# Kernel optimization log

Measured on AMD Instinct MI355X. Metric: run time of the kernel, lower is better.

## Reference

```python
import jax, jax.numpy as jnp
import numpy as np

C = 256; HEADS = 8; LEVELS = 4; POINTS = 4; D = C // HEADS
SPATIAL = np.array([[96, 96], [48, 48], [24, 24], [12, 12]], dtype=np.int32)  # (H, W) per level
AREAS = SPATIAL[:, 0] * SPATIAL[:, 1]
HW = int(AREAS.sum())  # 12240
LSI = np.concatenate([[0], np.cumsum(AREAS)[:-1]]).astype(np.int32)
N = 1; Q = HW


def setup_inputs() -> dict:
    key = jax.random.key(0)
    ks = jax.random.split(key, 12)
    s = 0.02
    return {
        "query": jax.random.normal(ks[0], (N, Q, C), jnp.float32),
        "reference_points": jax.random.uniform(ks[1], (N, Q, LEVELS, 2), jnp.float32),
        "input_flatten": jax.random.normal(ks[2], (N, HW, C), jnp.float32),
        "input_spatial_shapes": jnp.asarray(SPATIAL),
        "input_level_start_index": jnp.asarray(LSI),
        "W_off": jax.random.normal(ks[3], (C, HEADS * LEVELS * POINTS * 2), jnp.float32) * s,
        "b_off": jax.random.normal(ks[4], (HEADS * LEVELS * POINTS * 2,), jnp.float32) * s,
        "W_attn": jax.random.normal(ks[5], (C, HEADS * LEVELS * POINTS), jnp.float32) * s,
        "b_attn": jax.random.normal(ks[6], (HEADS * LEVELS * POINTS,), jnp.float32) * s,
        "W_val": jax.random.normal(ks[7], (C, C), jnp.float32) * (1.0 / np.sqrt(C)),
        "b_val": jax.random.normal(ks[8], (C,), jnp.float32) * s,
        "W_out": jax.random.normal(ks[9], (C, C), jnp.float32) * (1.0 / np.sqrt(C)),
        "b_out": jax.random.normal(ks[10], (C,), jnp.float32) * s,
    }


def _ms_deform_attn(query, reference_points, input_flatten, sp, lsi,
                    W_off, b_off, W_attn, b_attn, W_val, b_val, W_out, b_out):
    n, q, c = query.shape
    hw = input_flatten.shape[1]
    # value projection -> [N, Hd, HW, D]
    value = (input_flatten @ W_val + b_val).reshape(n, hw, HEADS, D).transpose(0, 2, 1, 3)
    # sampling offsets [N,Q,Hd,L,P,2]
    off = (query @ W_off + b_off).reshape(n, q, HEADS, LEVELS, POINTS, 2)
    # attention weights softmaxed over L*P (done inside the fused CUDA kernel)
    attn = jax.nn.softmax((query @ W_attn + b_attn).reshape(n, q, HEADS, LEVELS * POINTS), axis=-1)
    attn = attn.reshape(n, q, HEADS, LEVELS, POINTS)
    # normalized sampling locations (reference_points last dim == 2 branch)
    norm = jnp.stack([sp[:, 1], sp[:, 0]], -1).astype(query.dtype)  # (W, H) per level
    loc = reference_points[:, :, None, :, None, :] + off / norm[None, None, None, :, None, :]
    Hl = sp[:, 0][None, None, None, :, None]
    Wl = sp[:, 1][None, None, None, :, None]
    start = lsi[None, None, None, :, None]
    # grid_sample-style (align_corners=False) pixel coordinates
    x = loc[..., 0] * Wl - 0.5
    y = loc[..., 1] * Hl - 0.5
    x0 = jnp.floor(x); y0 = jnp.floor(y)
    lx = x - x0; ly = y - y0
    x0i = x0.astype(jnp.int32); y0i = y0.astype(jnp.int32)

    def gather(yi, xi):
        valid = (xi >= 0) & (xi < Wl) & (yi >= 0) & (yi < Hl)
        idx = jnp.where(valid, start + yi * Wl + xi, 0)  # [N,Q,Hd,L,P]
        idx_t = idx.transpose(0, 2, 1, 3, 4).reshape(n, HEADS, q * LEVELS * POINTS, 1)
        g = jnp.take_along_axis(value, idx_t, axis=2)  # [N,Hd,Q*L*P,D]
        g = g.reshape(n, HEADS, q, LEVELS, POINTS, D)
        return g * valid.transpose(0, 2, 1, 3, 4)[..., None]

    def w(a):
        return a.transpose(0, 2, 1, 3, 4)[..., None]  # [N,Hd,Q,L,P,1]

    sampled = (gather(y0i, x0i) * w((1 - ly) * (1 - lx))
               + gather(y0i, x0i + 1) * w((1 - ly) * lx)
               + gather(y0i + 1, x0i) * w(ly * (1 - lx))
               + gather(y0i + 1, x0i + 1) * w(ly * lx))  # [N,Hd,Q,L,P,D]
    out = jnp.einsum('nhqlpd,nqhlp->nqhd', sampled, attn).reshape(n, q, c)
    return out @ W_out + b_out


def reference(query, reference_points, input_flatten, input_spatial_shapes, input_level_start_index,
              W_off, b_off, W_attn, b_attn, W_val, b_val, W_out, b_out):
    return _ms_deform_attn(query, reference_points, input_flatten,
                           input_spatial_shapes, input_level_start_index,
                           W_off, b_off, W_attn, b_attn, W_val, b_val, W_out, b_out)
```

## Files before the change

kernel.cpp:

```cpp
#include <hip/hip_runtime.h>

#define QTOT 12240
#define KD   256

typedef float f32x4 __attribute__((ext_vector_type(4)));
typedef short s16x8 __attribute__((ext_vector_type(8)));
typedef unsigned short ushort_t;

__device__ __forceinline__ unsigned short f2b(float x) {
    union { float f; unsigned u; } c; c.f = x;
    unsigned r = c.u + 0x7fffu + ((c.u >> 16) & 1u);
    return (unsigned short)(r >> 16);
}
__device__ __forceinline__ int swz(int row, int kb) { return row * 512 + (kb ^ ((row & 7) << 4)); }

__global__ __launch_bounds__(256) void prep(
    const float* __restrict__ W_val, const float* __restrict__ W_off,
    const float* __restrict__ W_attn, const float* __restrict__ W_out,
    const float* __restrict__ b_off, const float* __restrict__ b_attn,
    ushort_t* __restrict__ WvT, ushort_t* __restrict__ WcT,
    ushort_t* __restrict__ WoT, float* __restrict__ bcomb)
{
    int id = blockIdx.x * 256 + threadIdx.x;
    if (id < 65536) { int n = id >> 8, k = id & 255; WvT[id] = f2b(W_val[k * 256 + n]); }
    else if (id < 163840) {
        int t = id - 65536; int n = t >> 8, k = t & 255;
        float v = (n < 256) ? W_off[k * 256 + n] : W_attn[k * 128 + (n - 256)];
        WcT[t] = f2b(v);
    } else if (id < 229376) {
        int t = id - 163840; int n = t >> 8, k = t & 255;
        WoT[t] = f2b(W_out[k * 256 + n]);
    } else if (id < 229760) {
        int t = id - 229376; bcomb[t] = (t < 256) ? b_off[t] : b_attn[t - 256];
    }
}

__global__ __launch_bounds__(256) void gemm1(
    const float* __restrict__ inflat, const float* __restrict__ query,
    const ushort_t* __restrict__ WvT, const ushort_t* __restrict__ WcT,
    const float* __restrict__ b_val, const float* __restrict__ bcomb,
    ushort_t* __restrict__ projb, ushort_t* __restrict__ offb,
    float* __restrict__ logitf)
{
    __shared__ char As[16384];
    const int b = blockIdx.x;
    const bool isval = b < 383;
    const int bm = (isval ? b : b - 383) * 32;
    const float* A = isval ? inflat : query;
    const ushort_t* WT = isval ? WvT : WcT;
    const int nc = isval ? 4 : 6;

    const int tid = threadIdx.x, lane = tid & 63, wave = tid >> 6;
    const int lr = lane & 15, g8 = (lane >> 4) * 8;

    {
        const int row = tid >> 3, c0 = (tid & 7) * 32;
        const int grow = bm + row;
        if (grow < QTOT) {
            const float4* src = (const float4*)(A + (size_t)grow * KD + c0);
#pragma unroll
            for (int j = 0; j < 4; ++j) {
                float4 f0 = src[j * 2 + 0], f1 = src[j * 2 + 1];
                s16x8 v;
                v[0] = f2b(f0.x); v[1] = f2b(f0.y); v[2] = f2b(f0.z); v[3] = f2b(f0.w);
                v[4] = f2b(f1.x); v[5] = f2b(f1.y); v[6] = f2b(f1.z); v[7] = f2b(f1.w);
                *(s16x8*)(As + swz(row, (c0 + j * 8) * 2)) = v;
            }
        } else {
            s16x8 z = (s16x8)0;
#pragma unroll
            for (int j = 0; j < 4; ++j)
                *(s16x8*)(As + swz(row, (c0 + j * 8) * 2)) = z;
        }
    }
    __syncthreads();

    const int rg = (lane >> 4) * 4;

    for (int c = 0; c < nc; ++c) {
        const int col = c * 64 + wave * 16 + lr;
        s16x8 bfr[8];
        {
            const ushort_t* bp = WT + (size_t)col * KD + g8;
#pragma unroll
            for (int kc = 0; kc < 8; ++kc) bfr[kc] = *(const s16x8*)(bp + kc * 32);
        }
        f32x4 acc[2];
        acc[0] = (f32x4)0.f; acc[1] = (f32x4)0.f;
#pragma unroll
        for (int kc = 0; kc < 8; ++kc) {
            const int kb = (kc * 32 + g8) * 2;
            s16x8 a0 = *(const s16x8*)(As + swz(lr,      kb));
            s16x8 a1 = *(const s16x8*)(As + swz(16 + lr, kb));
            acc[0] = __builtin_amdgcn_mfma_f32_16x16x32_bf16(a0, bfr[kc], acc[0], 0, 0, 0);
            acc[1] = __builtin_amdgcn_mfma_f32_16x16x32_bf16(a1, bfr[kc], acc[1], 0, 0, 0);
        }
        const float bb = isval ? b_val[col] : bcomb[col];
#pragma unroll
        for (int mf = 0; mf < 2; ++mf)
#pragma unroll
            for (int rr = 0; rr < 4; ++rr) {
                const int row = bm + mf * 16 + rg + rr;
                if (row >= QTOT) continue;
                const float v = acc[mf][rr] + bb;
                if (isval)          projb[(size_t)row * 256 + col] = f2b(v);
                else if (col < 256) offb [(size_t)row * 256 + col] = f2b(v);
                else                logitf[(size_t)row * 128 + col - 256] = v;
            }
    }
}

__global__ __launch_bounds__(512) void sample_o(
    const float* __restrict__ rp, const ushort_t* __restrict__ offb,
    const float* __restrict__ logitf, const ushort_t* __restrict__ projb,
    const int* __restrict__ sp, const int* __restrict__ lsi,
    const ushort_t* __restrict__ WoT, const float* __restrict__ b_out,
    float* __restrict__ out)
{
    __shared__ int   s_idx[1024][4];
    __shared__ float s_w[1024][4];
    __shared__ char  outp[16384];

    const int bid = blockIdx.x;
    const int bm = bid * 32;
    const int tid = threadIdx.x;

    for (int sb = 0; sb < 4; ++sb) {
        const int qloc0 = sb * 8;
#pragma unroll
        for (int rep = 0; rep < 2; ++rep) {
            const int task = rep * 512 + tid;
            const int ql = task >> 7, t = task & 127;
            const int l = (t >> 2) & 3;
            int q = bm + qloc0 + ql;
            const int qc = (q < QTOT) ? q : (QTOT - 1);

            float logit = logitf[(size_t)qc * 128 + t];
            float mx = logit;
#pragma unroll
            for (int d = 1; d < 16; d <<= 1) mx = fmaxf(mx, __shfl_xor(mx, d));
            float e = __expf(logit - mx);
            float s = e;
#pragma unroll
            for (int d = 1; d < 16; d <<= 1) s += __shfl_xor(s, d);
            const float aw = e / s;

            const unsigned opk = *(const unsigned*)&offb[(size_t)qc * 256 + t * 2];
            const float ox = __uint_as_float(opk << 16);
            const float oy = __uint_as_float(opk & 0xffff0000u);

            const int Hl = sp[l * 2], Wl = sp[l * 2 + 1], st = lsi[l];
            const float rx = rp[((size_t)qc * 4 + l) * 2 + 0];
            const float ry = rp[((size_t)qc * 4 + l) * 2 + 1];

            const float x = rx * (float)Wl + ox - 0.5f;
            const float y = ry * (float)Hl + oy - 0.5f;
            const float xf = floorf(x), yf = floorf(y);
            const int x0 = (int)xf, y0 = (int)yf;
            const float lx = x - xf, ly = y - yf;

            const bool vx0 = (x0 >= 0) && (x0 < Wl);
            const bool vx1 = (x0 + 1 >= 0) && (x0 + 1 < Wl);
            const bool vy0 = (y0 >= 0) && (y0 < Hl);
            const bool vy1 = (y0 + 1 >= 0) && (y0 + 1 < Hl);

            s_w[task][0] = (vx0 && vy0) ? aw * (1.f - ly) * (1.f - lx) : 0.f;
            s_w[task][1] = (vx1 && vy0) ? aw * (1.f - ly) * lx         : 0.f;
            s_w[task][2] = (vx0 && vy1) ? aw * ly * (1.f - lx)         : 0.f;
            s_w[task][3] = (vx1 && vy1) ? aw * ly * lx                 : 0.f;
            s_idx[task][0] = (vx0 && vy0) ? (st + y0 * Wl + x0) * 512           : 0;
            s_idx[task][1] = (vx1 && vy0) ? (st + y0 * Wl + x0 + 1) * 512       : 0;
            s_idx[task][2] = (vx0 && vy1) ? (st + (y0 + 1) * Wl + x0) * 512     : 0;
            s_idx[task][3] = (vx1 && vy1) ? (st + (y0 + 1) * Wl + x0 + 1) * 512 : 0;
        }
        __syncthreads();

        {
            const int t = tid & 127, qlA = tid >> 7;
            const int h = t >> 4, pq = (t >> 2) & 3, c8 = t & 3;
            const char* basec = (const char*)projb + (h * 32 + c8 * 8) * 2;

            float aA[8] = {0,0,0,0,0,0,0,0};
            float aB[8] = {0,0,0,0,0,0,0,0};
#pragma unroll
            for (int l = 0; l < 4; ++l) {
                const int slotA = (qlA << 7)       + h * 16 + l * 4 + pq;
                const int slotB = ((qlA + 4) << 7) + h * 16 + l * 4 + pq;
                const int4   iA = *(const int4*)s_idx[slotA];
                const float4 wA = *(const float4*)s_w[slotA];
                const int4   iB = *(const int4*)s_idx[slotB];
                const float4 wB = *(const float4*)s_w[slotB];
#pragma unroll
                for (int c = 0; c < 4; ++c) {
                    const int   idA = (c == 0) ? iA.x : (c == 1) ? iA.y : (c == 2) ? iA.z : iA.w;
                    const float wwA = (c == 0) ? wA.x : (c == 1) ? wA.y : (c == 2) ? wA.z : wA.w;
                    const uint4 v = *(const uint4*)(basec + idA);
                    aA[0] += wwA * __uint_as_float(v.x << 16);
                    aA[1] += wwA * __uint_as_float(v.x & 0xffff0000u);
                    aA[2] += wwA * __uint_as_float(v.y << 16);
                    aA[3] += wwA * __uint_as_float(v.y & 0xffff0000u);
                    aA[4] += wwA * __uint_as_float(v.z << 16);
                    aA[5] += wwA * __uint_as_float(v.z & 0xffff0000u);
                    aA[6] += wwA * __uint_as_float(v.w << 16);
                    aA[7] += wwA * __uint_as_float(v.w & 0xffff0000u);
                }
#pragma unroll
                for (int c = 0; c < 4; ++c) {
                    const int   idB = (c == 0) ? iB.x : (c == 1) ? iB.y : (c == 2) ? iB.z : iB.w;
                    const float wwB = (c == 0) ? wB.x : (c == 1) ? wB.y : (c == 2) ? wB.z : wB.w;
                    const uint4 v = *(const uint4*)(basec + idB);
                    aB[0] += wwB * __uint_as_float(v.x << 16);
                    aB[1] += wwB * __uint_as_float(v.x & 0xffff0000u);
                    aB[2] += wwB * __uint_as_float(v.y << 16);
                    aB[3] += wwB * __uint_as_float(v.y & 0xffff0000u);
                    aB[4] += wwB * __uint_as_float(v.z << 16);
                    aB[5] += wwB * __uint_as_float(v.z & 0xffff0000u);
                    aB[6] += wwB * __uint_as_float(v.w << 16);
                    aB[7] += wwB * __uint_as_float(v.w & 0xffff0000u);
                }
            }
#pragma unroll
            for (int i = 0; i < 8; ++i) {
                aA[i] += __shfl_xor(aA[i], 4);  aA[i] += __shfl_xor(aA[i], 8);
                aB[i] += __shfl_xor(aB[i], 4);  aB[i] += __shfl_xor(aB[i], 8);
            }
            if (pq == 0) {
                const int colb = (h * 32 + c8 * 8) * 2;
                uint4 o;
                o.x = (unsigned)f2b(aA[0]) | ((unsigned)f2b(aA[1]) << 16);
                o.y = (unsigned)f2b(aA[2]) | ((unsigned)f2b(aA[3]) << 16);
                o.z = (unsigned)f2b(aA[4]) | ((unsigned)f2b(aA[5]) << 16);
                o.w = (unsigned)f2b(aA[6]) | ((unsigned)f2b(aA[7]) << 16);
                *(uint4*)(outp + swz(qloc0 + qlA, colb)) = o;
                o.x = (unsigned)f2b(aB[0]) | ((unsigned)f2b(aB[1]) << 16);
                o.y = (unsigned)f2b(aB[2]) | ((unsigned)f2b(aB[3]) << 16);
                o.z = (unsigned)f2b(aB[4]) | ((unsigned)f2b(aB[5]) << 16);
                o.w = (unsigned)f2b(aB[6]) | ((unsigned)f2b(aB[7]) << 16);
                *(uint4*)(outp + swz(qloc0 + qlA + 4, colb)) = o;
            }
        }
        __syncthreads();
    }

    const int lane = tid & 63, wave = tid >> 6;
    const int lr = lane & 15, g8 = (lane >> 4) * 8, rg = (lane >> 4) * 4;

    s16x8 bfr[2][8];
#pragma unroll
    for (int nf = 0; nf < 2; ++nf) {
        const ushort_t* bp = WoT + (size_t)(wave * 32 + nf * 16 + lr) * KD + g8;
#pragma unroll
        for (int kc = 0; kc < 8; ++kc) bfr[nf][kc] = *(const s16x8*)(bp + kc * 32);
    }

    f32x4 acc[2][2];
    acc[0][0] = (f32x4)0.f; acc[0][1] = (f32x4)0.f;
    acc[1][0] = (f32x4)0.f; acc[1][1] = (f32x4)0.f;
#pragma unroll
    for (int kc = 0; kc < 8; ++kc) {
        const int kb = (kc * 32 + g8) * 2;
        s16x8 a0 = *(const s16x8*)(outp + swz(lr,      kb));
        s16x8 a1 = *(const s16x8*)(outp + swz(16 + lr, kb));
        acc[0][0] = __builtin_amdgcn_mfma_f32_16x16x32_bf16(a0, bfr[0][kc], acc[0][0], 0, 0, 0);
        acc[1][0] = __builtin_amdgcn_mfma_f32_16x16x32_bf16(a1, bfr[0][kc], acc[1][0], 0, 0, 0);
        acc[0][1] = __builtin_amdgcn_mfma_f32_16x16x32_bf16(a0, bfr[1][kc], acc[0][1], 0, 0, 0);
        acc[1][1] = __builtin_amdgcn_mfma_f32_16x16x32_bf16(a1, bfr[1][kc], acc[1][1], 0, 0, 0);
    }

#pragma unroll
    for (int nf = 0; nf < 2; ++nf) {
        const int col = wave * 32 + nf * 16 + lr;
        const float bb = b_out[col];
#pragma unroll
        for (int mf = 0; mf < 2; ++mf)
#pragma unroll
            for (int rr = 0; rr < 4; ++rr) {
                const int row = bm + mf * 16 + rg + rr;
                if (row < QTOT) out[(size_t)row * 256 + col] = acc[mf][nf][rr] + bb;
            }
    }
}

extern "C" void kernel_launch(void* const* d_in, const int* in_sizes, int n_in,
                              void* d_out, int out_size, void* d_ws, size_t ws_size,
                              hipStream_t stream) {
    const float* query  = (const float*)d_in[0];
    const float* rp     = (const float*)d_in[1];
    const float* inflat = (const float*)d_in[2];
    const int*   sp     = (const int*)d_in[3];
    const int*   lsi    = (const int*)d_in[4];
    const float* W_off  = (const float*)d_in[5];
    const float* b_off  = (const float*)d_in[6];
    const float* W_attn = (const float*)d_in[7];
    const float* b_attn = (const float*)d_in[8];
    const float* W_val  = (const float*)d_in[9];
    const float* b_val  = (const float*)d_in[10];
    const float* W_out  = (const float*)d_in[11];
    const float* b_out  = (const float*)d_in[12];
    float* out = (float*)d_out;

    char* ws = (char*)d_ws;
    ushort_t* projb  = (ushort_t*)ws; ws += (size_t)QTOT * 256 * 2;
    ushort_t* offb   = (ushort_t*)ws; ws += (size_t)QTOT * 256 * 2;
    float*    logitf = (float*)ws;    ws += (size_t)QTOT * 128 * 4;
    ushort_t* WvT    = (ushort_t*)ws; ws += 65536 * 2;
    ushort_t* WcT    = (ushort_t*)ws; ws += 98304 * 2;
    ushort_t* WoT    = (ushort_t*)ws; ws += 65536 * 2;
    float*    bcomb  = (float*)ws;    ws += 384 * 4;

    prep<<<dim3(898), dim3(256), 0, stream>>>(W_val, W_off, W_attn, W_out, b_off, b_attn,
                                              WvT, WcT, WoT, bcomb);

    gemm1<<<dim3(766), dim3(256), 0, stream>>>(inflat, query, WvT, WcT, b_val, bcomb,
                                               projb, offb, logitf);

    sample_o<<<dim3(383), dim3(512), 0, stream>>>(rp, offb, logitf, projb, sp, lsi,
                                                  WoT, b_out, out);
}
```

Before: 82.24 us.

## Split sampling from output GEMM into separate kernels with finer-grained blocks

```diff
diff --git a/kernel.cpp b/kernel.cpp
--- a/kernel.cpp
+++ b/kernel.cpp
@@ -5,6 +5,7 @@
 
 typedef float f32x4 __attribute__((ext_vector_type(4)));
 typedef short s16x8 __attribute__((ext_vector_type(8)));
+typedef short s16x4 __attribute__((ext_vector_type(4)));
 typedef unsigned short ushort_t;
 
 __device__ __forceinline__ unsigned short f2b(float x) {
@@ -54,23 +55,18 @@
     const int lr = lane & 15, g8 = (lane >> 4) * 8;
 
     {
-        const int row = tid >> 3, c0 = (tid & 7) * 32;
-        const int grow = bm + row;
-        if (grow < QTOT) {
-            const float4* src = (const float4*)(A + (size_t)grow * KD + c0);
-#pragma unroll
-            for (int j = 0; j < 4; ++j) {
-                float4 f0 = src[j * 2 + 0], f1 = src[j * 2 + 1];
-                s16x8 v;
-                v[0] = f2b(f0.x); v[1] = f2b(f0.y); v[2] = f2b(f0.z); v[3] = f2b(f0.w);
-                v[4] = f2b(f1.x); v[5] = f2b(f1.y); v[6] = f2b(f1.z); v[7] = f2b(f1.w);
-                *(s16x8*)(As + swz(row, (c0 + j * 8) * 2)) = v;
-            }
-        } else {
-            s16x8 z = (s16x8)0;
-#pragma unroll
-            for (int j = 0; j < 4; ++j)
-                *(s16x8*)(As + swz(row, (c0 + j * 8) * 2)) = z;
+        const float4* srcb = (const float4*)(A + (size_t)bm * KD);
+        const int rem_rows = QTOT - bm;
+#pragma unroll
+        for (int j = 0; j < 8; ++j) {
+            const int f4i = j * 256 + tid;
+            const int row = f4i >> 6;
+            const int colb = (f4i & 63) * 8;
+            float4 f = make_float4(0.f, 0.f, 0.f, 0.f);
+            if (row < rem_rows) f = srcb[f4i];
+            s16x4 v;
+            v[0] = f2b(f.x); v[1] = f2b(f.y); v[2] = f2b(f.z); v[3] = f2b(f.w);
+            *(s16x4*)(As + swz(row, colb)) = v;
         }
     }
     __syncthreads();
@@ -110,173 +106,172 @@
     }
 }
 
-__global__ __launch_bounds__(512) void sample_o(
+__global__ __launch_bounds__(256) void sample5(
     const float* __restrict__ rp, const ushort_t* __restrict__ offb,
     const float* __restrict__ logitf, const ushort_t* __restrict__ projb,
     const int* __restrict__ sp, const int* __restrict__ lsi,
-    const ushort_t* __restrict__ WoT, const float* __restrict__ b_out,
-    float* __restrict__ out)
+    ushort_t* __restrict__ outpre)
 {
-    __shared__ int   s_idx[1024][4];
-    __shared__ float s_w[1024][4];
-    __shared__ char  outp[16384];
-
-    const int bid = blockIdx.x;
-    const int bm = bid * 32;
+    const int q0 = blockIdx.x * 4;
     const int tid = threadIdx.x;
 
-    for (int sb = 0; sb < 4; ++sb) {
-        const int qloc0 = sb * 8;
-#pragma unroll
-        for (int rep = 0; rep < 2; ++rep) {
-            const int task = rep * 512 + tid;
-            const int ql = task >> 7, t = task & 127;
-            const int l = (t >> 2) & 3;
-            int q = bm + qloc0 + ql;
-            const int qc = (q < QTOT) ? q : (QTOT - 1);
-
-            float logit = logitf[(size_t)qc * 128 + t];
-            float mx = logit;
-#pragma unroll
-            for (int d = 1; d < 16; d <<= 1) mx = fmaxf(mx, __shfl_xor(mx, d));
-            float e = __expf(logit - mx);
-            float s = e;
-#pragma unroll
-            for (int d = 1; d < 16; d <<= 1) s += __shfl_xor(s, d);
-            const float aw = e / s;
-
-            const unsigned opk = *(const unsigned*)&offb[(size_t)qc * 256 + t * 2];
-            const float ox = __uint_as_float(opk << 16);
-            const float oy = __uint_as_float(opk & 0xffff0000u);
-
-            const int Hl = sp[l * 2], Wl = sp[l * 2 + 1], st = lsi[l];
-            const float rx = rp[((size_t)qc * 4 + l) * 2 + 0];
-            const float ry = rp[((size_t)qc * 4 + l) * 2 + 1];
-
-            const float x = rx * (float)Wl + ox - 0.5f;
-            const float y = ry * (float)Hl + oy - 0.5f;
-            const float xf = floorf(x), yf = floorf(y);
-            const int x0 = (int)xf, y0 = (int)yf;
-            const float lx = x - xf, ly = y - yf;
-
-            const bool vx0 = (x0 >= 0) && (x0 < Wl);
-            const bool vx1 = (x0 + 1 >= 0) && (x0 + 1 < Wl);
-            const bool vy0 = (y0 >= 0) && (y0 < Hl);
-            const bool vy1 = (y0 + 1 >= 0) && (y0 + 1 < Hl);
-
-            s_w[task][0] = (vx0 && vy0) ? aw * (1.f - ly) * (1.f - lx) : 0.f;
-            s_w[task][1] = (vx1 && vy0) ? aw * (1.f - ly) * lx         : 0.f;
-            s_w[task][2] = (vx0 && vy1) ? aw * ly * (1.f - lx)         : 0.f;
-            s_w[task][3] = (vx1 && vy1) ? aw * ly * lx                 : 0.f;
-            s_idx[task][0] = (vx0 && vy0) ? (st + y0 * Wl + x0) * 512           : 0;
-            s_idx[task][1] = (vx1 && vy0) ? (st + y0 * Wl + x0 + 1) * 512       : 0;
-            s_idx[task][2] = (vx0 && vy1) ? (st + (y0 + 1) * Wl + x0) * 512     : 0;
-            s_idx[task][3] = (vx1 && vy1) ? (st + (y0 + 1) * Wl + x0 + 1) * 512 : 0;
-        }
-        __syncthreads();
-
+    __shared__ int   s_idx[512][4];
+    __shared__ float s_w[512][4];
+
+#pragma unroll
+    for (int rep = 0; rep < 2; ++rep) {
+        const int task = rep * 256 + tid;
+        const int ql = task >> 7, t = task & 127;
+        const int l = (t >> 2) & 3;
+        const int q = q0 + ql;
+
+        float logit = logitf[(size_t)q * 128 + t];
+        float mx = logit;
+#pragma unroll
+        for (int d = 1; d < 16; d <<= 1) mx = fmaxf(mx, __shfl_xor(mx, d));
+        float e = __expf(logit - mx);
+        float s = e;
+#pragma unroll
+        for (int d = 1; d < 16; d <<= 1) s += __shfl_xor(s, d);
+        const float aw = e / s;
+
+        const unsigned opk = *(const unsigned*)&offb[(size_t)q * 256 + t * 2];
+        const float ox = __uint_as_float(opk << 16);
+        const float oy = __uint_as_float(opk & 0xffff0000u);
+
+        const int Hl = sp[l * 2], Wl = sp[l * 2 + 1], st = lsi[l];
+        const float rx = rp[((size_t)q * 4 + l) * 2 + 0];
+        const float ry = rp[((size_t)q * 4 + l) * 2 + 1];
+
+        const float x = rx * (float)Wl + ox - 0.5f;
+        const float y = ry * (float)Hl + oy - 0.5f;
+        const float xf = floorf(x), yf = floorf(y);
+        const int x0 = (int)xf, y0 = (int)yf;
+        const float lx = x - xf, ly = y - yf;
+
+        const bool vx0 = (x0 >= 0) && (x0 < Wl);
+        const bool vx1 = (x0 + 1 >= 0) && (x0 + 1 < Wl);
+        const bool vy0 = (y0 >= 0) && (y0 < Hl);
+        const bool vy1 = (y0 + 1 >= 0) && (y0 + 1 < Hl);
+
+        s_w[task][0] = (vx0 && vy0) ? aw * (1.f - ly) * (1.f - lx) : 0.f;
+        s_w[task][1] = (vx1 && vy0) ? aw * (1.f - ly) * lx         : 0.f;
+        s_w[task][2] = (vx0 && vy1) ? aw * ly * (1.f - lx)         : 0.f;
+        s_w[task][3] = (vx1 && vy1) ? aw * ly * lx                 : 0.f;
+        s_idx[task][0] = (vx0 && vy0) ? (st + y0 * Wl + x0) * 512           : 0;
+        s_idx[task][1] = (vx1 && vy0) ? (st + y0 * Wl + x0 + 1) * 512       : 0;
+        s_idx[task][2] = (vx0 && vy1) ? (st + (y0 + 1) * Wl + x0) * 512     : 0;
+        s_idx[task][3] = (vx1 && vy1) ? (st + (y0 + 1) * Wl + x0 + 1) * 512 : 0;
+    }
+    __syncthreads();
+
+    const int t = tid & 127, qlA = tid >> 7;
+    const int h = t >> 4, pq = (t >> 2) & 3, c8 = t & 3;
+    const char* basec = (const char*)projb + (h * 32 + c8 * 8) * 2;
+
+    float aA[8] = {0,0,0,0,0,0,0,0};
+    float aB[8] = {0,0,0,0,0,0,0,0};
+#pragma unroll
+    for (int l = 0; l < 4; ++l) {
+        const int slotA = (qlA << 7)       + h * 16 + l * 4 + pq;
+        const int slotB = ((qlA + 2) << 7) + h * 16 + l * 4 + pq;
+        const int4   iA = *(const int4*)s_idx[slotA];
+        const float4 wA = *(const float4*)s_w[slotA];
+        const int4   iB = *(const int4*)s_idx[slotB];
+        const float4 wB = *(const float4*)s_w[slotB];
+#pragma unroll
+        for (int c = 0; c < 4; ++c) {
+            const int   idA = (c == 0) ? iA.x : (c == 1) ? iA.y : (c == 2) ? iA.z : iA.w;
+            const float wwA = (c == 0) ? wA.x : (c == 1) ? wA.y : (c == 2) ? wA.z : wA.w;
+            const uint4 v = *(const uint4*)(basec + idA);
+            aA[0] += wwA * __uint_as_float(v.x << 16);
+            aA[1] += wwA * __uint_as_float(v.x & 0xffff0000u);
+            aA[2] += wwA * __uint_as_float(v.y << 16);
+            aA[3] += wwA * __uint_as_float(v.y & 0xffff0000u);
+            aA[4] += wwA * __uint_as_float(v.z << 16);
+            aA[5] += wwA * __uint_as_float(v.z & 0xffff0000u);
+            aA[6] += wwA * __uint_as_float(v.w << 16);
+            aA[7] += wwA * __uint_as_float(v.w & 0xffff0000u);
+        }
+#pragma unroll
+        for (int c = 0; c < 4; ++c) {
+            const int   idB = (c == 0) ? iB.x : (c == 1) ? iB.y : (c == 2) ? iB.z : iB.w;
+            const float wwB = (c == 0) ? wB.x : (c == 1) ? wB.y : (c == 2) ? wB.z : wB.w;
+            const uint4 v = *(const uint4*)(basec + idB);
+            aB[0] += wwB * __uint_as_float(v.x << 16);
+            aB[1] += wwB * __uint_as_float(v.x & 0xffff0000u);
+            aB[2] += wwB * __uint_as_float(v.y << 16);
+            aB[3] += wwB * __uint_as_float(v.y & 0xffff0000u);
+            aB[4] += wwB * __uint_as_float(v.z << 16);
+            aB[5] += wwB * __uint_as_float(v.z & 0xffff0000u);
+            aB[6] += wwB * __uint_as_float(v.w << 16);
+            aB[7] += wwB * __uint_as_float(v.w & 0xffff0000u);
+        }
+    }
+#pragma unroll
+    for (int i = 0; i < 8; ++i) {
+        aA[i] += __shfl_xor(aA[i], 4);  aA[i] += __shfl_xor(aA[i], 8);
+        aB[i] += __shfl_xor(aB[i], 4);  aB[i] += __shfl_xor(aB[i], 8);
+    }
+    if (pq == 0) {
+        const int colo = h * 32 + c8 * 8;
+        uint4 o;
+        o.x = (unsigned)f2b(aA[0]) | ((unsigned)f2b(aA[1]) << 16);
+        o.y = (unsigned)f2b(aA[2]) | ((unsigned)f2b(aA[3]) << 16);
+        o.z = (unsigned)f2b(aA[4]) | ((unsigned)f2b(aA[5]) << 16);
+        o.w = (unsigned)f2b(aA[6]) | ((unsigned)f2b(aA[7]) << 16);
+        *(uint4*)&outpre[(size_t)(q0 + qlA) * 256 + colo] = o;
+        o.x = (unsigned)f2b(aB[0]) | ((unsigned)f2b(aB[1]) << 16);
+        o.y = (unsigned)f2b(aB[2]) | ((unsigned)f2b(aB[3]) << 16);
+        o.z = (unsigned)f2b(aB[4]) | ((unsigned)f2b(aB[5]) << 16);
+        o.w = (unsigned)f2b(aB[6]) | ((unsigned)f2b(aB[7]) << 16);
+        *(uint4*)&outpre[(size_t)(q0 + qlA + 2) * 256 + colo] = o;
+    }
+}
+
+__global__ __launch_bounds__(256) void gemm_o(
+    const ushort_t* __restrict__ Ab, const ushort_t* __restrict__ WoT,
+    const float* __restrict__ b_out, float* __restrict__ out)
+{
+    const int bm = blockIdx.x * 32;
+    const int tid = threadIdx.x, lane = tid & 63, wave = tid >> 6;
+    const int lr = lane & 15, g8 = (lane >> 4) * 8;
+    const int rg = (lane >> 4) * 4;
+
+    const ushort_t* ap0;
+    const ushort_t* ap1;
+    {
+        int r0 = bm + lr;      if (r0 >= QTOT) r0 = QTOT - 1;
+        int r1 = bm + 16 + lr; if (r1 >= QTOT) r1 = QTOT - 1;
+        ap0 = Ab + (size_t)r0 * KD + g8;
+        ap1 = Ab + (size_t)r1 * KD + g8;
+    }
+
+#pragma unroll
+    for (int c = 0; c < 4; ++c) {
+        const int col = c * 64 + wave * 16 + lr;
+        s16x8 bfr[8];
         {
-            const int t = tid & 127, qlA = tid >> 7;
-            const int h = t >> 4, pq = (t >> 2) & 3, c8 = t & 3;
-            const char* basec = (const char*)projb + (h * 32 + c8 * 8) * 2;
-
-            float aA[8] = {0,0,0,0,0,0,0,0};
-            float aB[8] = {0,0,0,0,0,0,0,0};
-#pragma unroll
-            for (int l = 0; l < 4; ++l) {
-                const int slotA = (qlA << 7)       + h * 16 + l * 4 + pq;
-                const int slotB = ((qlA + 4) << 7) + h * 16 + l * 4 + pq;
-                const int4   iA = *(const int4*)s_idx[slotA];
-                const float4 wA = *(const float4*)s_w[slotA];
-                const int4   iB = *(const int4*)s_idx[slotB];
-                const float4 wB = *(const float4*)s_w[slotB];
-#pragma unroll
-                for (int c = 0; c < 4; ++c) {
-                    const int   idA = (c == 0) ? iA.x : (c == 1) ? iA.y : (c == 2) ? iA.z : iA.w;
-                    const float wwA = (c == 0) ? wA.x : (c == 1) ? wA.y : (c == 2) ? wA.z : wA.w;
-                    const uint4 v = *(const uint4*)(basec + idA);
-                    aA[0] += wwA * __uint_as_float(v.x << 16);
-                    aA[1] += wwA * __uint_as_float(v.x & 0xffff0000u);
-                    aA[2] += wwA * __uint_as_float(v.y << 16);
-                    aA[3] += wwA * __uint_as_float(v.y & 0xffff0000u);
-                    aA[4] += wwA * __uint_as_float(v.z << 16);
-                    aA[5] += wwA * __uint_as_float(v.z & 0xffff0000u);
-                    aA[6] += wwA * __uint_as_float(v.w << 16);
-                    aA[7] += wwA * __uint_as_float(v.w & 0xffff0000u);
-                }
-#pragma unroll
-                for (int c = 0; c < 4; ++c) {
-                    const int   idB = (c == 0) ? iB.x : (c == 1) ? iB.y : (c == 2) ? iB.z : iB.w;
-                    const float wwB = (c == 0) ? wB.x : (c == 1) ? wB.y : (c == 2) ? wB.z : wB.w;
-                    const uint4 v = *(const uint4*)(basec + idB);
-                    aB[0] += wwB * __uint_as_float(v.x << 16);
-                    aB[1] += wwB * __uint_as_float(v.x & 0xffff0000u);
-                    aB[2] += wwB * __uint_as_float(v.y << 16);
-                    aB[3] += wwB * __uint_as_float(v.y & 0xffff0000u);
-                    aB[4] += wwB * __uint_as_float(v.z << 16);
-                    aB[5] += wwB * __uint_as_float(v.z & 0xffff0000u);
-                    aB[6] += wwB * __uint_as_float(v.w << 16);
-                    aB[7] += wwB * __uint_as_float(v.w & 0xffff0000u);
-                }
-            }
-#pragma unroll
-            for (int i = 0; i < 8; ++i) {
-                aA[i] += __shfl_xor(aA[i], 4);  aA[i] += __shfl_xor(aA[i], 8);
-                aB[i] += __shfl_xor(aB[i], 4);  aB[i] += __shfl_xor(aB[i], 8);
-            }
-            if (pq == 0) {
-                const int colb = (h * 32 + c8 * 8) * 2;
-                uint4 o;
-                o.x = (unsigned)f2b(aA[0]) | ((unsigned)f2b(aA[1]) << 16);
-                o.y = (unsigned)f2b(aA[2]) | ((unsigned)f2b(aA[3]) << 16);
-                o.z = (unsigned)f2b(aA[4]) | ((unsigned)f2b(aA[5]) << 16);
-                o.w = (unsigned)f2b(aA[6]) | ((unsigned)f2b(aA[7]) << 16);
-                *(uint4*)(outp + swz(qloc0 + qlA, colb)) = o;
-                o.x = (unsigned)f2b(aB[0]) | ((unsigned)f2b(aB[1]) << 16);
-                o.y = (unsigned)f2b(aB[2]) | ((unsigned)f2b(aB[3]) << 16);
-                o.z = (unsigned)f2b(aB[4]) | ((unsigned)f2b(aB[5]) << 16);
-                o.w = (unsigned)f2b(aB[6]) | ((unsigned)f2b(aB[7]) << 16);
-                *(uint4*)(outp + swz(qloc0 + qlA + 4, colb)) = o;
-            }
-        }
-        __syncthreads();
-    }
-
-    const int lane = tid & 63, wave = tid >> 6;
-    const int lr = lane & 15, g8 = (lane >> 4) * 8, rg = (lane >> 4) * 4;
-
-    s16x8 bfr[2][8];
-#pragma unroll
-    for (int nf = 0; nf < 2; ++nf) {
-        const ushort_t* bp = WoT + (size_t)(wave * 32 + nf * 16 + lr) * KD + g8;
-#pragma unroll
-        for (int kc = 0; kc < 8; ++kc) bfr[nf][kc] = *(const s16x8*)(bp + kc * 32);
-    }
-
-    f32x4 acc[2][2];
-    acc[0][0] = (f32x4)0.f; acc[0][1] = (f32x4)0.f;
-    acc[1][0] = (f32x4)0.f; acc[1][1] = (f32x4)0.f;
-#pragma unroll
-    for (int kc = 0; kc < 8; ++kc) {
-        const int kb = (kc * 32 + g8) * 2;
-        s16x8 a0 = *(const s16x8*)(outp + swz(lr,      kb));
-        s16x8 a1 = *(const s16x8*)(outp + swz(16 + lr, kb));
-        acc[0][0] = __builtin_amdgcn_mfma_f32_16x16x32_bf16(a0, bfr[0][kc], acc[0][0], 0, 0, 0);
-        acc[1][0] = __builtin_amdgcn_mfma_f32_16x16x32_bf16(a1, bfr[0][kc], acc[1][0], 0, 0, 0);
-        acc[0][1] = __builtin_amdgcn_mfma_f32_16x16x32_bf16(a0, bfr[1][kc], acc[0][1], 0, 0, 0);
-        acc[1][1] = __builtin_amdgcn_mfma_f32_16x16x32_bf16(a1, bfr[1][kc], acc[1][1], 0, 0, 0);
-    }
-
-#pragma unroll
-    for (int nf = 0; nf < 2; ++nf) {
-        const int col = wave * 32 + nf * 16 + lr;
+            const ushort_t* bp = WoT + (size_t)col * KD + g8;
+#pragma unroll
+            for (int kc = 0; kc < 8; ++kc) bfr[kc] = *(const s16x8*)(bp + kc * 32);
+        }
+        f32x4 acc[2];
+        acc[0] = (f32x4)0.f; acc[1] = (f32x4)0.f;
+#pragma unroll
+        for (int kc = 0; kc < 8; ++kc) {
+            s16x8 a0 = *(const s16x8*)(ap0 + kc * 32);
+            s16x8 a1 = *(const s16x8*)(ap1 + kc * 32);
+            acc[0] = __builtin_amdgcn_mfma_f32_16x16x32_bf16(a0, bfr[kc], acc[0], 0, 0, 0);
+            acc[1] = __builtin_amdgcn_mfma_f32_16x16x32_bf16(a1, bfr[kc], acc[1], 0, 0, 0);
+        }
         const float bb = b_out[col];
 #pragma unroll
         for (int mf = 0; mf < 2; ++mf)
 #pragma unroll
             for (int rr = 0; rr < 4; ++rr) {
                 const int row = bm + mf * 16 + rg + rr;
-                if (row < QTOT) out[(size_t)row * 256 + col] = acc[mf][nf][rr] + bb;
+                if (row < QTOT) out[(size_t)row * 256 + col] = acc[mf][rr] + bb;
             }
     }
 }
@@ -303,6 +298,7 @@
     ushort_t* projb  = (ushort_t*)ws; ws += (size_t)QTOT * 256 * 2;
     ushort_t* offb   = (ushort_t*)ws; ws += (size_t)QTOT * 256 * 2;
     float*    logitf = (float*)ws;    ws += (size_t)QTOT * 128 * 4;
+    ushort_t* outpre = (ushort_t*)ws; ws += (size_t)QTOT * 256 * 2;
     ushort_t* WvT    = (ushort_t*)ws; ws += 65536 * 2;
     ushort_t* WcT    = (ushort_t*)ws; ws += 98304 * 2;
     ushort_t* WoT    = (ushort_t*)ws; ws += 65536 * 2;
@@ -314,6 +310,7 @@
     gemm1<<<dim3(766), dim3(256), 0, stream>>>(inflat, query, WvT, WcT, b_val, bcomb,
                                                projb, offb, logitf);
 
-    sample_o<<<dim3(383), dim3(512), 0, stream>>>(rp, offb, logitf, projb, sp, lsi,
-                                                  WoT, b_out, out);
-}
+    sample5<<<dim3(3060), dim3(256), 0, stream>>>(rp, offb, logitf, projb, sp, lsi, outpre);
+
+    gemm_o<<<dim3(383), dim3(256), 0, stream>>>(outpre, WoT, b_out, out);
+}
```

Measured after the change: 69.72 us, median of 2. 1.18x faster.
